# Optimization experiments

Measured on AMD Instinct MI355X. Metric: run time of the kernel, lower is better.

Reference implementation:

```python
import jax, jax.numpy as jnp
import numpy as np

# --- constants matching init_kwargs ---
D = 768        # d_model (hidden)
H = 12         # attn heads
DK = D // H    # 64
F = 3072       # KANsize1
G = 5          # grid_size
K = 3          # spline_order
C = G + K      # spline coefficients per (out,in)
EPS = 1e-5
# efficient-kan grid: arange(-K, G+K+1)*h + grid_range[0], grid_range=[-1,1], h=2/G
GRID = jnp.arange(-K, G + K + 1, dtype=jnp.float32) * (2.0 / G) - 1.0  # (G+2K+1,)


def b_splines(x, grid, k):
    """x: (..., in) -> B-spline bases (..., in, G+K) via Cox-de Boor."""
    xe = x[..., None]
    bases = ((xe >= grid[:-1]) & (xe < grid[1:])).astype(x.dtype)
    for j in range(1, k + 1):
        bases = ((xe - grid[:-(j + 1)]) / (grid[j:-1] - grid[:-(j + 1)]) * bases[..., :-1]
                 + (grid[j + 1:] - xe) / (grid[j + 1:] - grid[1:-j]) * bases[..., 1:])
    return bases


def kan_linear(x, base_w, spline_w, scaler):
    # efficient-kan KANLinear: silu-base GEMM + scaled spline GEMM
    base = jnp.einsum('bsi,oi->bso', jax.nn.silu(x), base_w)
    B = b_splines(x, GRID, K)                      # (b, s, in, C)
    sw = spline_w * scaler[..., None]              # (out, in, C)
    spline = jnp.einsum('bsic,oic->bso', B, sw)
    return base + spline


def layernorm(x, g, b):
    m = jnp.mean(x, -1, keepdims=True)
    v = jnp.var(x, -1, keepdims=True)
    return (x - m) * jax.lax.rsqrt(v + EPS) * g + b


def setup_inputs() -> dict:
    key = jax.random.key(0)
    ks = jax.random.split(key, 12)
    Bt, S = 2, 2048
    x = jax.random.normal(ks[0], (Bt, S, D), jnp.float32)
    mask = jnp.ones((Bt, 1, 1, S), bool)  # accepted but unused, as in source
    s = 0.02
    return {
        'x': x, 'mask': mask,
        'ln1_g': jnp.ones((D,), jnp.float32), 'ln1_b': jnp.zeros((D,), jnp.float32),
        'wq': jax.random.normal(ks[1], (D, D), jnp.float32) * s, 'bq': jnp.zeros((D,), jnp.float32),
        'wk': jax.random.normal(ks[2], (D, D), jnp.float32) * s, 'bk': jnp.zeros((D,), jnp.float32),
        'wv': jax.random.normal(ks[3], (D, D), jnp.float32) * s, 'bv': jnp.zeros((D,), jnp.float32),
        'ln2_g': jnp.ones((D,), jnp.float32), 'ln2_b': jnp.zeros((D,), jnp.float32),
        'base_w1': jax.random.normal(ks[4], (F, D), jnp.float32) * s,
        'spline_w1': jax.random.normal(ks[5], (F, D, C), jnp.float32) * 0.1,
        'scaler1': jnp.ones((F, D), jnp.float32),
        'base_w2': jax.random.normal(ks[6], (D, F), jnp.float32) * s,
        'spline_w2': jax.random.normal(ks[7], (D, F, C), jnp.float32) * 0.1,
        'scaler2': jnp.ones((D, F), jnp.float32),
    }


def reference(x, mask, ln1_g, ln1_b, wq, bq, wk, bk, wv, bv, ln2_g, ln2_b,
              base_w1, spline_w1, scaler1, base_w2, spline_w2, scaler2):
    Bt, S, _ = x.shape
    # MultiHeadedAttention (pre-norm inside; mask unused in source; dropout=eval identity)
    xn = layernorm(x, ln1_g, ln1_b)
    q = (xn @ wq.T + bq).reshape(Bt, S, H, DK).transpose(0, 2, 1, 3)
    k = (xn @ wk.T + bk).reshape(Bt, S, H, DK).transpose(0, 2, 1, 3)
    v = (xn @ wv.T + bv).reshape(Bt, S, H, DK).transpose(0, 2, 1, 3)
    scores = jnp.einsum('bhqd,bhkd->bhqk', q, k) / jnp.sqrt(jnp.float32(DK))
    p = jax.nn.softmax(scores, axis=-1)
    attn = jnp.einsum('bhqk,bhkd->bhqd', p, v).transpose(0, 2, 1, 3).reshape(Bt, S, D)
    x = x + attn
    # SublayerConnection: x + KAN-FFN(norm(x))
    h = layernorm(x, ln2_g, ln2_b)
    h = kan_linear(h, base_w1, spline_w1, scaler1)
    h = kan_linear(h, base_w2, spline_w2, scaler2)
    return x + h
```

## Files before the change

### kernel.cpp

```cpp
#include <hip/hip_runtime.h>
#include <hip/hip_fp16.h>
#include <math.h>

#define DEV static __device__ __forceinline__

namespace {
constexpr int S  = 2048;
constexpr int D  = 768;
constexpr int Hh = 12;
constexpr int DK = 64;
constexpr int F  = 3072;
constexpr int Nn = 4096;
constexpr int FEAT = 9;
constexpr int K1   = D * FEAT;
constexpr int LDAB = 6912;
}

typedef _Float16 half8 __attribute__((ext_vector_type(8)));
typedef float f32x4 __attribute__((ext_vector_type(4)));

DEV void gld16(const void* g, void* l) {
    __builtin_amdgcn_global_load_lds((__attribute__((address_space(1))) void*)g,
                                     (__attribute__((address_space(3))) void*)l,
                                     16, 0, 0);
}

DEV int xcd_swz(int id, int nwg) {
    int q = nwg >> 3, r = nwg & 7;
    int xcd = id & 7, pos = id >> 3;
    return (xcd < r ? xcd * (q + 1) : r * (q + 1) + (xcd - r) * q) + pos;
}

DEV void features9(float xv, float* f) {
    f[0] = xv / (1.0f + __expf(-xv));
    float sp = (xv + 2.2f) * 2.5f;
    float fj = floorf(sp);
    int j = (int)fj;
    float u = sp - fj;
    float u2 = u * u, u3 = u2 * u;
    float omu = 1.0f - u;
    float b0 = (1.0f / 6.0f) * omu * omu * omu;
    float b1 = 0.5f * u3 - u2 + (2.0f / 3.0f);
    float b2 = -0.5f * u3 + 0.5f * u2 + 0.5f * u + (1.0f / 6.0f);
    float b3 = (1.0f / 6.0f) * u3;
#pragma unroll
    for (int m = 0; m < 8; ++m) {
        int d = j - m;
        f[1 + m] = (d == 3) ? b0 : (d == 2) ? b1 : (d == 1) ? b2 : (d == 0) ? b3 : 0.0f;
    }
}

__global__ __launch_bounds__(256) void ln16_kernel(const float* __restrict__ x,
                                                   const float* __restrict__ g,
                                                   const float* __restrict__ bta,
                                                   _Float16* __restrict__ y) {
    int row = blockIdx.x;
    const float* xr = x + (size_t)row * D;
    _Float16* yr = y + (size_t)row * D;
    int t = threadIdx.x;
    float v[3];
#pragma unroll
    for (int j = 0; j < 3; ++j) v[j] = xr[t + j * 256];
    float s = v[0] + v[1] + v[2];
#pragma unroll
    for (int o = 1; o < 64; o <<= 1) s += __shfl_xor(s, o, 64);
    __shared__ float red[4], red2[4];
    int wid = t >> 6;
    if ((t & 63) == 0) red[wid] = s;
    __syncthreads();
    float mean = (red[0] + red[1] + red[2] + red[3]) * (1.0f / 768.0f);
    float d0 = v[0] - mean, d1 = v[1] - mean, d2 = v[2] - mean;
    float sq = d0 * d0 + d1 * d1 + d2 * d2;
#pragma unroll
    for (int o = 1; o < 64; o <<= 1) sq += __shfl_xor(sq, o, 64);
    if ((t & 63) == 0) red2[wid] = sq;
    __syncthreads();
    float var = (red2[0] + red2[1] + red2[2] + red2[3]) * (1.0f / 768.0f);
    float rstd = rsqrtf(var + 1e-5f);
#pragma unroll
    for (int j = 0; j < 3; ++j) {
        int c = t + j * 256;
        yr[c] = (_Float16)((v[j] - mean) * rstd * g[c] + bta[c]);
    }
}

__global__ __launch_bounds__(256) void ln_feat(const float* __restrict__ xa,
                                               const float* __restrict__ xb,
                                               const float* __restrict__ g,
                                               const float* __restrict__ bta,
                                               _Float16* __restrict__ feat) {
    int row = blockIdx.x;
    const float* xar = xa + (size_t)row * D;
    const float* xbr = xb + (size_t)row * D;
    int t = threadIdx.x;
    float v[3];
#pragma unroll
    for (int j = 0; j < 3; ++j) v[j] = xar[t + j * 256] + xbr[t + j * 256];
    float s = v[0] + v[1] + v[2];
#pragma unroll
    for (int o = 1; o < 64; o <<= 1) s += __shfl_xor(s, o, 64);
    __shared__ float red[4], red2[4];
    __shared__ __align__(16) _Float16 fbuf[K1];
    int wid = t >> 6;
    if ((t & 63) == 0) red[wid] = s;
    __syncthreads();
    float mean = (red[0] + red[1] + red[2] + red[3]) * (1.0f / 768.0f);
    float d0 = v[0] - mean, d1 = v[1] - mean, d2 = v[2] - mean;
    float sq = d0 * d0 + d1 * d1 + d2 * d2;
#pragma unroll
    for (int o = 1; o < 64; o <<= 1) sq += __shfl_xor(sq, o, 64);
    if ((t & 63) == 0) red2[wid] = sq;
    __syncthreads();
    float var = (red2[0] + red2[1] + red2[2] + red2[3]) * (1.0f / 768.0f);
    float rstd = rsqrtf(var + 1e-5f);
#pragma unroll
    for (int j = 0; j < 3; ++j) {
        int c = t + j * 256;
        float y = (v[j] - mean) * rstd * g[c] + bta[c];
        float f[9];
        features9(y, f);
#pragma unroll
        for (int cc = 0; cc < 9; ++cc) fbuf[c * 9 + cc] = (_Float16)f[cc];
    }
    __syncthreads();
    _Float16* dst = feat + (size_t)row * K1;
    for (int i = t; i < K1 / 8; i += 256)
        *(half8*)(dst + i * 8) = *(const half8*)&fbuf[i * 8];
}

__global__ __launch_bounds__(256) void feat2_chunk(const _Float16* __restrict__ h1,
                                                   int c0,
                                                   _Float16* __restrict__ feat) {
    int row = blockIdx.x;
    int t = threadIdx.x;
    __shared__ __align__(16) _Float16 fbuf[K1];
    const _Float16* src = h1 + (size_t)row * F + c0;
#pragma unroll
    for (int j = 0; j < 3; ++j) {
        int ic = t + j * 256;
        float y = (float)src[ic];
        float f[9];
        features9(y, f);
#pragma unroll
        for (int cc = 0; cc < 9; ++cc) fbuf[ic * 9 + cc] = (_Float16)f[cc];
    }
    __syncthreads();
    _Float16* dst = feat + (size_t)row * K1;
    for (int i = t; i < K1 / 8; i += 256)
        *(half8*)(dst + i * 8) = *(const half8*)&fbuf[i * 8];
}

__global__ __launch_bounds__(256) void prep_w(const float* __restrict__ bw,
                                              const float* __restrict__ sw,
                                              const float* __restrict__ scal,
                                              _Float16* __restrict__ Wp,
                                              int INfull, int c0) {
    int o = blockIdx.y;
    int ic = blockIdx.x * 256 + threadIdx.x;
    size_t idx = (size_t)o * INfull + c0 + ic;
    float bwv = bw[idx];
    float sc  = scal[idx];
    float4 s0 = *(const float4*)(sw + idx * 8);
    float4 s1 = *(const float4*)(sw + idx * 8 + 4);
    _Float16* dst = Wp + ((size_t)o * 768 + ic) * 9;
    dst[0] = (_Float16)bwv;
    dst[1] = (_Float16)(s0.x * sc);
    dst[2] = (_Float16)(s0.y * sc);
    dst[3] = (_Float16)(s0.z * sc);
    dst[4] = (_Float16)(s0.w * sc);
    dst[5] = (_Float16)(s1.x * sc);
    dst[6] = (_Float16)(s1.y * sc);
    dst[7] = (_Float16)(s1.z * sc);
    dst[8] = (_Float16)(s1.w * sc);
}

__global__ __launch_bounds__(256) void prep_qkv(const float* __restrict__ wq,
                                                const float* __restrict__ wk,
                                                const float* __restrict__ wv,
                                                _Float16* __restrict__ Wh) {
    int idx = blockIdx.x * 256 + threadIdx.x;
    const int per = D * D;
    if (idx >= 3 * per) return;
    int z = idx / per, rem = idx - z * per;
    const float* w = (z == 0) ? wq : (z == 1) ? wk : wv;
    Wh[idx] = (_Float16)w[rem];
}

__global__ __launch_bounds__(256, 2) void qkv16(const _Float16* __restrict__ Xh,
                                                const _Float16* __restrict__ Wh,
                                                const float* __restrict__ bq,
                                                const float* __restrict__ bk,
                                                const float* __restrict__ bv,
                                                _Float16* __restrict__ q,
                                                _Float16* __restrict__ k,
                                                _Float16* __restrict__ v) {
    int nb = gridDim.x, mb = gridDim.y;
    int nwg = nb * mb * gridDim.z;
    int id = blockIdx.x + nb * (blockIdx.y + mb * blockIdx.z);
    int id2 = xcd_swz(id, nwg);
    int z = id2 / (nb * mb);
    int rem = id2 % (nb * mb);
    int m0 = (rem % mb) * 128, o0 = (rem / mb) * 128;

    const _Float16* W = Wh + (size_t)z * D * D;
    const float* bias = (z == 0) ? bq : (z == 1) ? bk : bv;
    _Float16* out     = (z == 0) ? q  : (z == 1) ? k  : v;

    __shared__ __align__(16) _Float16 As[128][72];
    int t = threadIdx.x;
    int l = t & 63, w = t >> 6;
    int wr = (w >> 1) * 64, wc = (w & 1) * 64;
    int lm = l & 15, lk = (l >> 4) * 8;
    int srow = t >> 1, sh = t & 1;

    f32x4 acc[4][4];
#pragma unroll
    for (int a = 0; a < 4; ++a)
#pragma unroll
        for (int b = 0; b < 4; ++b)
#pragma unroll
            for (int c = 0; c < 4; ++c) acc[a][b][c] = 0.0f;

    const _Float16* bp0 = W + (size_t)(o0 + wc + lm) * D + lk;

    for (int kt = 0; kt < D / 64; ++kt) {
        half8 ar[4];
#pragma unroll
        for (int i = 0; i < 4; ++i)
            ar[i] = *(const half8*)(Xh + (size_t)(m0 + srow) * D + kt * 64 + sh * 32 + i * 8);
        __syncthreads();
#pragma unroll
        for (int i = 0; i < 4; ++i)
            *(half8*)&As[srow][sh * 32 + i * 8] = ar[i];
        __syncthreads();
        half8 bfr[2][4];
#pragma unroll
        for (int kc = 0; kc < 2; ++kc)
#pragma unroll
            for (int nf = 0; nf < 4; ++nf)
                bfr[kc][nf] = *(const half8*)(bp0 + (size_t)nf * 16 * D + kt * 64 + kc * 32);
#pragma unroll
        for (int kc = 0; kc < 2; ++kc) {
            half8 a_[4];
#pragma unroll
            for (int mf = 0; mf < 4; ++mf)
                a_[mf] = *(const half8*)&As[wr + mf * 16 + lm][kc * 32 + lk];
#pragma unroll
            for (int mf = 0; mf < 4; ++mf)
#pragma unroll
                for (int nf = 0; nf < 4; ++nf)
                    acc[mf][nf] = __builtin_amdgcn_mfma_f32_16x16x32_f16(a_[mf], bfr[kc][nf], acc[mf][nf], 0, 0, 0);
        }
    }
    int r0 = m0 + wr + (l >> 4) * 4;
    int c0 = o0 + wc + lm;
#pragma unroll
    for (int mf = 0; mf < 4; ++mf)
#pragma unroll
        for (int nf = 0; nf < 4; ++nf) {
            int col = c0 + nf * 16;
            int hh = col >> 6, dd = col & 63;
            float bv_ = bias[col];
#pragma unroll
            for (int r = 0; r < 4; ++r) {
                int n = r0 + mf * 16 + r;
                int b = n >> 11, ss = n & 2047;
                out[(((size_t)(b * Hh + hh) * S + ss) * DK + dd)] = (_Float16)(acc[mf][nf][r] + bv_);
            }
        }
}

__global__ __launch_bounds__(512) void attn16(const _Float16* __restrict__ q16,
                                              const _Float16* __restrict__ k16,
                                              const _Float16* __restrict__ v16,
                                              float* __restrict__ attno) {
    int nwg = gridDim.x * gridDim.y;
    int id = blockIdx.x + gridDim.x * blockIdx.y;
    int id2 = xcd_swz(id, nwg);
    int bh = id2 / gridDim.x;
    int q0 = (id2 % gridDim.x) * 128;

    int t = threadIdx.x;
    int l = t & 63, w = t >> 6;
    int lm = l & 15, lk = (l >> 4) * 8;
    int wr = w * 16;

    __shared__ __align__(16) _Float16 Qs[128][72];
    __shared__ __align__(16) _Float16 Ps[128][72];
    __shared__ __align__(16) _Float16 Ks[64][72];
    __shared__ __align__(16) _Float16 Vt[64][72];

    const _Float16* qb = q16 + ((size_t)bh * S + q0) * DK;
    const _Float16* kb = k16 + (size_t)bh * S * DK;
    const _Float16* vb = v16 + (size_t)bh * S * DK;

    {
        int row = t >> 2, dg = t & 3;
        half8 h0 = *(const half8*)(qb + row * DK + dg * 16);
        half8 h1 = *(const half8*)(qb + row * DK + dg * 16 + 8);
#pragma unroll
        for (int j = 0; j < 8; ++j) { h0[j] = h0[j] * (_Float16)0.125f; h1[j] = h1[j] * (_Float16)0.125f; }
        *(half8*)&Qs[row][dg * 16] = h0;
        *(half8*)&Qs[row][dg * 16 + 8] = h1;
    }

    float m_[4], l_[4];
    f32x4 oacc[4];
#pragma unroll
    for (int r = 0; r < 4; ++r) { m_[r] = -INFINITY; l_[r] = 0.0f; }
#pragma unroll
    for (int nf = 0; nf < 4; ++nf)
#pragma unroll
        for (int r = 0; r < 4; ++r) oacc[nf][r] = 0.0f;

    for (int kt = 0; kt < S / 64; ++kt) {
        __syncthreads();
        {
            int tt = t & 255;
            int key = tt & 63, dg = tt >> 6;
            if (t < 256) {
                const _Float16* kr = kb + ((size_t)kt * 64 + key) * DK + dg * 16;
                half8 k0 = *(const half8*)(kr);
                half8 k1 = *(const half8*)(kr + 8);
                *(half8*)&Ks[key][dg * 16] = k0;
                *(half8*)&Ks[key][dg * 16 + 8] = k1;
            } else {
                const _Float16* vr = vb + ((size_t)kt * 64 + key) * DK + dg * 16;
                half8 v0 = *(const half8*)(vr);
                half8 v1 = *(const half8*)(vr + 8);
#pragma unroll
                for (int j = 0; j < 8; ++j) {
                    Vt[dg * 16 + j][key] = v0[j];
                    Vt[dg * 16 + 8 + j][key] = v1[j];
                }
            }
        }
        __syncthreads();

        f32x4 sc[4];
#pragma unroll
        for (int nf = 0; nf < 4; ++nf)
#pragma unroll
            for (int r = 0; r < 4; ++r) sc[nf][r] = 0.0f;
        __builtin_amdgcn_s_setprio(1);
#pragma unroll
        for (int kc = 0; kc < 2; ++kc) {
            half8 aq = *(const half8*)&Qs[wr + lm][kc * 32 + lk];
#pragma unroll
            for (int nf = 0; nf < 4; ++nf) {
                half8 bk8 = *(const half8*)&Ks[nf * 16 + lm][kc * 32 + lk];
                sc[nf] = __builtin_amdgcn_mfma_f32_16x16x32_f16(aq, bk8, sc[nf], 0, 0, 0);
            }
        }
        __builtin_amdgcn_s_setprio(0);
        float pmax[4];
#pragma unroll
        for (int r = 0; r < 4; ++r) {
            pmax[r] = fmaxf(fmaxf(sc[0][r], sc[1][r]), fmaxf(sc[2][r], sc[3][r]));
#pragma unroll
            for (int mk = 1; mk < 16; mk <<= 1)
                pmax[r] = fmaxf(pmax[r], __shfl_xor(pmax[r], mk, 64));
        }
        float corr[4], rs[4];
#pragma unroll
        for (int r = 0; r < 4; ++r) {
            float mnew = fmaxf(m_[r], pmax[r]);
            corr[r] = __expf(m_[r] - mnew);
            m_[r] = mnew;
            rs[r] = 0.0f;
        }
#pragma unroll
        for (int nf = 0; nf < 4; ++nf)
#pragma unroll
            for (int r = 0; r < 4; ++r) {
                float p = __expf(sc[nf][r] - m_[r]);
                sc[nf][r] = p;
                rs[r] += p;
            }
#pragma unroll
        for (int r = 0; r < 4; ++r) {
#pragma unroll
            for (int mk = 1; mk < 16; mk <<= 1)
                rs[r] += __shfl_xor(rs[r], mk, 64);
            l_[r] = l_[r] * corr[r] + rs[r];
        }
        int pr = wr + (l >> 4) * 4;
#pragma unroll
        for (int nf = 0; nf < 4; ++nf)
#pragma unroll
            for (int r = 0; r < 4; ++r)
                Ps[pr + r][nf * 16 + lm] = (_Float16)sc[nf][r];
#pragma unroll
        for (int nf = 0; nf < 4; ++nf)
#pragma unroll
            for (int r = 0; r < 4; ++r) oacc[nf][r] *= corr[r];
        __builtin_amdgcn_s_setprio(1);
#pragma unroll
        for (int kc = 0; kc < 2; ++kc) {
            half8 ap = *(const half8*)&Ps[wr + lm][kc * 32 + lk];
#pragma unroll
            for (int nf = 0; nf < 4; ++nf) {
                half8 bv8 = *(const half8*)&Vt[nf * 16 + lm][kc * 32 + lk];
                oacc[nf] = __builtin_amdgcn_mfma_f32_16x16x32_f16(ap, bv8, oacc[nf], 0, 0, 0);
            }
        }
        __builtin_amdgcn_s_setprio(0);
    }
    int b = bh / Hh, hh = bh % Hh;
    int pr = wr + (l >> 4) * 4;
#pragma unroll
    for (int r = 0; r < 4; ++r) {
        float inv = 1.0f / l_[r];
        float* orow = attno + ((size_t)b * S + q0 + pr + r) * D + hh * DK;
#pragma unroll
        for (int nf = 0; nf < 4; ++nf)
            orow[nf * 16 + lm] = oacc[nf][r] * inv;
    }
}

template <int KS, bool TOF16>
__global__ __launch_bounds__(256) void kan_gemm(const _Float16* __restrict__ A,
                                                const _Float16* __restrict__ B,
                                                _Float16* __restrict__ out16,
                                                float* __restrict__ out32,
                                                int O, int accum) {
    __shared__ __align__(16) _Float16 Al[128 * 64];
    __shared__ __align__(16) _Float16 Bl[128 * 64];
    int nb = gridDim.x, mb = gridDim.y;
    int nwg = nb * mb * gridDim.z;
    int id = blockIdx.x + nb * (blockIdx.y + mb * blockIdx.z);
    int id2 = xcd_swz(id, nwg);
    int slot = id2 / (nb * mb);
    int rem = id2 % (nb * mb);
    int m0 = (rem % mb) * 128, o0 = (rem / mb) * 128;

    int t = threadIdx.x;
    int l = t & 63, w = t >> 6;
    int wr = (w >> 1) * 64, wc = (w & 1) * 64;
    int lm = l & 15, lk = (l >> 4) * 8;

    const _Float16* Ab = A + (size_t)slot * KS * 64;
    const _Float16* Bb = B + (size_t)slot * KS * 64;
    int srow = l >> 3, scol = (l & 7) * 8;

    f32x4 acc[4][4];
#pragma unroll
    for (int a = 0; a < 4; ++a)
#pragma unroll
        for (int b = 0; b < 4; ++b)
#pragma unroll
            for (int c = 0; c < 4; ++c) acc[a][b][c] = 0.0f;

    for (int kt = 0; kt < KS; ++kt) {
        if (kt) __syncthreads();
        size_t kofs = (size_t)kt * 64 + scol;
#pragma unroll
        for (int j = 0; j < 4; ++j) {
            int row = w * 32 + j * 8;
            gld16(Ab + (size_t)(m0 + row + srow) * LDAB + kofs, &Al[row * 64]);
            gld16(Bb + (size_t)(o0 + row + srow) * LDAB + kofs, &Bl[row * 64]);
        }
        __syncthreads();
#pragma unroll
        for (int kc = 0; kc < 2; ++kc) {
            half8 af[4], bf[4];
#pragma unroll
            for (int mf = 0; mf < 4; ++mf)
                af[mf] = *(const half8*)&Al[(wr + mf * 16 + lm) * 64 + kc * 32 + lk];
#pragma unroll
            for (int nf = 0; nf < 4; ++nf)
                bf[nf] = *(const half8*)&Bl[(wc + nf * 16 + lm) * 64 + kc * 32 + lk];
#pragma unroll
            for (int mf = 0; mf < 4; ++mf)
#pragma unroll
                for (int nf = 0; nf < 4; ++nf)
                    acc[mf][nf] = __builtin_amdgcn_mfma_f32_16x16x32_f16(af[mf], bf[nf], acc[mf][nf], 0, 0, 0);
        }
    }
    int r0 = m0 + wr + (l >> 4) * 4;
    int c0 = o0 + wc + lm;
#pragma unroll
    for (int mf = 0; mf < 4; ++mf)
#pragma unroll
        for (int nf = 0; nf < 4; ++nf)
#pragma unroll
            for (int r = 0; r < 4; ++r) {
                int row = r0 + mf * 16 + r;
                int col = c0 + nf * 16;
                if constexpr (TOF16) {
                    out16[(size_t)row * O + col] = (_Float16)acc[mf][nf][r];
                } else {
                    float* po = out32 + ((size_t)slot * Nn + row) * O + col;
                    float vv = acc[mf][nf][r];
                    if (accum) vv += *po;
                    *po = vv;
                }
            }
}

__global__ __launch_bounds__(256) void reduce4(const float* __restrict__ part,
                                               const float* __restrict__ x,
                                               const float* __restrict__ attno,
                                               float* __restrict__ out) {
    int i = blockIdx.x * 256 + threadIdx.x;
    const size_t ND4 = (size_t)Nn * D / 4;
    if (i >= (int)ND4) return;
    const float4* p0 = (const float4*)part;
    const float4* p1 = p0 + ND4;
    const float4* p2 = p1 + ND4;
    const float4* p3 = p2 + ND4;
    float4 a = p0[i], b = p1[i], c = p2[i], d = p3[i];
    float4 xe = ((const float4*)x)[i], at = ((const float4*)attno)[i];
    float4 o;
    o.x = a.x + b.x + c.x + d.x + xe.x + at.x;
    o.y = a.y + b.y + c.y + d.y + xe.y + at.y;
    o.z = a.z + b.z + c.z + d.z + xe.z + at.z;
    o.w = a.w + b.w + c.w + d.w + xe.w + at.w;
    ((float4*)out)[i] = o;
}

extern "C" void kernel_launch(void* const* d_in, const int* in_sizes, int n_in,
                              void* d_out, int out_size, void* d_ws, size_t ws_size,
                              hipStream_t stream) {
    const float* x    = (const float*)d_in[0];
    const float* ln1g = (const float*)d_in[2];
    const float* ln1b = (const float*)d_in[3];
    const float* wq   = (const float*)d_in[4];
    const float* bq   = (const float*)d_in[5];
    const float* wk   = (const float*)d_in[6];
    const float* bk   = (const float*)d_in[7];
    const float* wv   = (const float*)d_in[8];
    const float* bv   = (const float*)d_in[9];
    const float* ln2g = (const float*)d_in[10];
    const float* ln2b = (const float*)d_in[11];
    const float* bw1  = (const float*)d_in[12];
    const float* sw1  = (const float*)d_in[13];
    const float* sc1  = (const float*)d_in[14];
    const float* bw2  = (const float*)d_in[15];
    const float* sw2  = (const float*)d_in[16];
    const float* sc2  = (const float*)d_in[17];

    const size_t ND = (size_t)Nn * D;
    char* base = (char*)d_ws;
    _Float16* featbuf = (_Float16*)base;
    _Float16* q16 = featbuf;
    _Float16* k16 = featbuf + ND;
    _Float16* v16 = featbuf + 2 * ND;
    char* p = base + (size_t)Nn * K1 * 2;
    float* attno = (float*)p;            p += ND * 4;
    _Float16* h1h = (_Float16*)p;        p += (size_t)Nn * F * 2;
    char* R3 = p;
    _Float16* Wp1 = (_Float16*)R3;
    _Float16* xnh = (_Float16*)(R3 + 42467328);
    _Float16* Wh  = (_Float16*)(R3 + 48758784);
    float* part   = (float*)R3;
    char* R4 = R3 + 52297728;
    _Float16* Wp2c = (_Float16*)R4;

    ln16_kernel<<<Nn, 256, 0, stream>>>(x, ln1g, ln1b, xnh);
    prep_qkv<<<(3 * D * D + 255) / 256, 256, 0, stream>>>(wq, wk, wv, Wh);
    qkv16<<<dim3(D / 128, Nn / 128, 3), 256, 0, stream>>>(xnh, Wh, bq, bk, bv, q16, k16, v16);
    attn16<<<dim3(S / 128, 2 * Hh), 512, 0, stream>>>(q16, k16, v16, attno);
    prep_w<<<dim3(3, F), 256, 0, stream>>>(bw1, sw1, sc1, Wp1, D, 0);
    ln_feat<<<Nn, 256, 0, stream>>>(x, attno, ln2g, ln2b, featbuf);
    kan_gemm<108, true><<<dim3(F / 128, Nn / 128, 1), 256, 0, stream>>>(
        featbuf, Wp1, h1h, nullptr, F, 0);
    for (int c = 0; c < 4; ++c) {
        prep_w<<<dim3(3, D), 256, 0, stream>>>(bw2, sw2, sc2, Wp2c, F, c * 768);
        feat2_chunk<<<Nn, 256, 0, stream>>>(h1h, c * 768, featbuf);
        kan_gemm<27, false><<<dim3(D / 128, Nn / 128, 4), 256, 0, stream>>>(
            featbuf, Wp2c, nullptr, part, D, c > 0);
    }
    reduce4<<<(int)(ND / 4 / 256), 256, 0, stream>>>(part, x, attno, (float*)d_out);
}
```

Baseline: 1.164 ms.

## Double-buffer KAN GEMM LDS tiles with XOR swizzle and drop XCD remap

```diff
diff --git a/kernel.cpp b/kernel.cpp
--- a/kernel.cpp
+++ b/kernel.cpp
@@ -194,14 +194,7 @@
                                                 _Float16* __restrict__ q,
                                                 _Float16* __restrict__ k,
                                                 _Float16* __restrict__ v) {
-    int nb = gridDim.x, mb = gridDim.y;
-    int nwg = nb * mb * gridDim.z;
-    int id = blockIdx.x + nb * (blockIdx.y + mb * blockIdx.z);
-    int id2 = xcd_swz(id, nwg);
-    int z = id2 / (nb * mb);
-    int rem = id2 % (nb * mb);
-    int m0 = (rem % mb) * 128, o0 = (rem / mb) * 128;
-
+    int z = blockIdx.z;
     const _Float16* W = Wh + (size_t)z * D * D;
     const float* bias = (z == 0) ? bq : (z == 1) ? bk : bv;
     _Float16* out     = (z == 0) ? q  : (z == 1) ? k  : v;
@@ -209,6 +202,7 @@
     __shared__ __align__(16) _Float16 As[128][72];
     int t = threadIdx.x;
     int l = t & 63, w = t >> 6;
+    int m0 = blockIdx.y * 128, o0 = blockIdx.x * 128;
     int wr = (w >> 1) * 64, wc = (w & 1) * 64;
     int lm = l & 15, lk = (l >> 4) * 8;
     int srow = t >> 1, sh = t & 1;
@@ -419,29 +413,24 @@
 }
 
 template <int KS, bool TOF16>
-__global__ __launch_bounds__(256) void kan_gemm(const _Float16* __restrict__ A,
-                                                const _Float16* __restrict__ B,
-                                                _Float16* __restrict__ out16,
-                                                float* __restrict__ out32,
-                                                int O, int accum) {
-    __shared__ __align__(16) _Float16 Al[128 * 64];
-    __shared__ __align__(16) _Float16 Bl[128 * 64];
-    int nb = gridDim.x, mb = gridDim.y;
-    int nwg = nb * mb * gridDim.z;
-    int id = blockIdx.x + nb * (blockIdx.y + mb * blockIdx.z);
-    int id2 = xcd_swz(id, nwg);
-    int slot = id2 / (nb * mb);
-    int rem = id2 % (nb * mb);
-    int m0 = (rem % mb) * 128, o0 = (rem / mb) * 128;
-
+__global__ __launch_bounds__(256, 2) void kan_gemm(const _Float16* __restrict__ A,
+                                                   const _Float16* __restrict__ B,
+                                                   _Float16* __restrict__ out16,
+                                                   float* __restrict__ out32,
+                                                   int O, int accum) {
+    __shared__ __align__(16) _Float16 Al[2][128 * 64];
+    __shared__ __align__(16) _Float16 Bl[2][128 * 64];
     int t = threadIdx.x;
     int l = t & 63, w = t >> 6;
+    int m0 = blockIdx.y * 128, o0 = blockIdx.x * 128;
+    int slot = blockIdx.z;
     int wr = (w >> 1) * 64, wc = (w & 1) * 64;
-    int lm = l & 15, lk = (l >> 4) * 8;
+    int lm = l & 15, lkq = l >> 4;
 
     const _Float16* Ab = A + (size_t)slot * KS * 64;
     const _Float16* Bb = B + (size_t)slot * KS * 64;
-    int srow = l >> 3, scol = (l & 7) * 8;
+    int srow = l >> 3;
+    int schunk = ((l & 7) ^ srow) * 8;
 
     f32x4 acc[4][4];
 #pragma unroll
@@ -451,32 +440,55 @@
 #pragma unroll
             for (int c = 0; c < 4; ++c) acc[a][b][c] = 0.0f;
 
-    for (int kt = 0; kt < KS; ++kt) {
-        if (kt) __syncthreads();
-        size_t kofs = (size_t)kt * 64 + scol;
+    auto stage = [&](int kt, int bu) {
+        size_t kofs = (size_t)kt * 64 + schunk;
 #pragma unroll
         for (int j = 0; j < 4; ++j) {
             int row = w * 32 + j * 8;
-            gld16(Ab + (size_t)(m0 + row + srow) * LDAB + kofs, &Al[row * 64]);
-            gld16(Bb + (size_t)(o0 + row + srow) * LDAB + kofs, &Bl[row * 64]);
-        }
-        __syncthreads();
+            gld16(Ab + (size_t)(m0 + row + srow) * LDAB + kofs, &Al[bu][row * 64]);
+            gld16(Bb + (size_t)(o0 + row + srow) * LDAB + kofs, &Bl[bu][row * 64]);
+        }
+    };
+
+    stage(0, 0);
+
+    for (int kt = 0; kt < KS; ++kt) {
+        int cur = kt & 1;
+        if (kt + 1 < KS) {
+            stage(kt + 1, cur ^ 1);
+            asm volatile("s_waitcnt vmcnt(8)" ::: "memory");
+        } else {
+            asm volatile("s_waitcnt vmcnt(0)" ::: "memory");
+        }
+        __builtin_amdgcn_sched_barrier(0);
+        __builtin_amdgcn_s_barrier();
+        __builtin_amdgcn_sched_barrier(0);
+
+        const _Float16* Ac = &Al[cur][0];
+        const _Float16* Bc = &Bl[cur][0];
 #pragma unroll
         for (int kc = 0; kc < 2; ++kc) {
+            int cw = (((kc * 4 + lkq) ^ (lm & 7)) * 8);
             half8 af[4], bf[4];
 #pragma unroll
             for (int mf = 0; mf < 4; ++mf)
-                af[mf] = *(const half8*)&Al[(wr + mf * 16 + lm) * 64 + kc * 32 + lk];
+                af[mf] = *(const half8*)&Ac[(wr + mf * 16 + lm) * 64 + cw];
 #pragma unroll
             for (int nf = 0; nf < 4; ++nf)
-                bf[nf] = *(const half8*)&Bl[(wc + nf * 16 + lm) * 64 + kc * 32 + lk];
+                bf[nf] = *(const half8*)&Bc[(wc + nf * 16 + lm) * 64 + cw];
+            __builtin_amdgcn_s_setprio(1);
 #pragma unroll
             for (int mf = 0; mf < 4; ++mf)
 #pragma unroll
                 for (int nf = 0; nf < 4; ++nf)
                     acc[mf][nf] = __builtin_amdgcn_mfma_f32_16x16x32_f16(af[mf], bf[nf], acc[mf][nf], 0, 0, 0);
-        }
-    }
+            __builtin_amdgcn_s_setprio(0);
+        }
+        __builtin_amdgcn_sched_barrier(0);
+        __builtin_amdgcn_s_barrier();
+        __builtin_amdgcn_sched_barrier(0);
+    }
+
     int r0 = m0 + wr + (l >> 4) * 4;
     int c0 = o0 + wc + lm;
 #pragma unroll
```

Measured after the change: 1.149 ms. About the same (-1.3%).
